# Kernel optimization log

Hardware: AMD Instinct MI355X
Metric: run time of the kernel (lower is better)

The kernel has to match this reference:

```python
import jax, jax.numpy as jnp
import numpy as np

B = 262144          # batch size
NUM_CLASSES = 1000  # number of classes in `classes` dict
CODE_LEN = 512      # length of each binary codeword in class_to_coding


def setup_inputs() -> dict:
    key = jax.random.key(0)
    k1, k2, k3 = jax.random.split(key, 3)
    output = jax.random.randint(k1, (B,), 0, NUM_CLASSES, dtype=jnp.int64 if jax.config.jax_enable_x64 else jnp.int32)
    target = jax.random.randint(k2, (B,), 0, NUM_CLASSES, dtype=output.dtype)
    # classes + class_to_coding fused into one [num_classes, code_len] binary table
    codebook = (jax.random.uniform(k3, (NUM_CLASSES, CODE_LEN)) > 0.5).astype(jnp.float32)
    return {"output": output, "target": target, "codebook": codebook}


def reference(output, target, codebook):
    # Vectorized equivalent of the per-sample Python loop:
    #   dist_i = sum(codebook[pred_i] != codebook[gt_i]); loss = mean_i dist_i
    pred_codes = codebook[output]   # [B, CODE_LEN]
    gt_codes = codebook[target]     # [B, CODE_LEN]
    dists = jnp.sum(pred_codes != gt_codes, axis=-1).astype(jnp.float32)  # [B]
    return jnp.mean(dists)
```

## Files before the change

kernel.cpp:

```cpp
#include <hip/hip_runtime.h>
#include <stdint.h>

#define B_SIZE        262144
#define NUM_CLASSES   1000
#define CODE_LEN      512
#define WORDS_PER_ROW 16
#define PACKED_WORDS  (NUM_CLASSES * WORDS_PER_ROW)
#define CHUNKS        (NUM_CLASSES * 4)
#define HAM_BLOCKS    512
#define SAMPLES_PER_BLOCK (B_SIZE / HAM_BLOCKS)

__global__ __launch_bounds__(256) void pack_kernel(
        const float* __restrict__ codebook,
        uint32_t* __restrict__ packed,
        unsigned long long* __restrict__ accum,
        unsigned int* __restrict__ done) {
    int tid = blockIdx.x * blockDim.x + threadIdx.x;
    if (tid == 0) { *accum = 0ull; *done = 0u; }
    if (tid < NUM_CLASSES * CODE_LEN) {
        float x = codebook[tid];
        unsigned long long m = __ballot(x > 0.5f);
        if ((tid & 31) == 0) {
            packed[tid >> 5] = (uint32_t)(m >> (threadIdx.x & 32));
        }
    }
}

__global__ __launch_bounds__(256) void hamming_kernel(
        const int* __restrict__ output,
        const int* __restrict__ target,
        const uint32_t* __restrict__ packed,
        unsigned long long* __restrict__ accum,
        unsigned int* __restrict__ done,
        float* __restrict__ out) {
    __shared__ uint4 lds[CHUNKS];
    __shared__ unsigned int wsum[4];

    const uint4* pk4 = (const uint4*)packed;
    #pragma unroll
    for (int it = 0; it < 16; it++) {
        int g = threadIdx.x + 256 * it;
        if (g < CHUNKS) {
            int r = g >> 2, k = g & 3;
            lds[(r << 2) + ((k + (r >> 2)) & 3)] = pk4[g];
        }
    }
    __syncthreads();

    int base = blockIdx.x * SAMPLES_PER_BLOCK + threadIdx.x;
    int i0 = base, i1 = base + 256;
    int o0 = output[i0], t0 = target[i0];
    int o1 = output[i1], t1 = target[i1];

    uint4 ao[4], at[4], bo[4], bt[4];
    int so0 = (o0 >> 2) & 3, st0 = (t0 >> 2) & 3;
    int so1 = (o1 >> 2) & 3, st1 = (t1 >> 2) & 3;
    #pragma unroll
    for (int k = 0; k < 4; k++) ao[k] = lds[(o0 << 2) + ((k + so0) & 3)];
    #pragma unroll
    for (int k = 0; k < 4; k++) at[k] = lds[(t0 << 2) + ((k + st0) & 3)];
    #pragma unroll
    for (int k = 0; k < 4; k++) bo[k] = lds[(o1 << 2) + ((k + so1) & 3)];
    #pragma unroll
    for (int k = 0; k < 4; k++) bt[k] = lds[(t1 << 2) + ((k + st1) & 3)];

    unsigned int sum = 0;
    #pragma unroll
    for (int k = 0; k < 4; k++) {
        sum += __popc(ao[k].x ^ at[k].x) + __popc(ao[k].y ^ at[k].y)
             + __popc(ao[k].z ^ at[k].z) + __popc(ao[k].w ^ at[k].w);
        sum += __popc(bo[k].x ^ bt[k].x) + __popc(bo[k].y ^ bt[k].y)
             + __popc(bo[k].z ^ bt[k].z) + __popc(bo[k].w ^ bt[k].w);
    }

    #pragma unroll
    for (int off = 32; off > 0; off >>= 1)
        sum += __shfl_down(sum, off, 64);
    if ((threadIdx.x & 63) == 0)
        wsum[threadIdx.x >> 6] = sum;
    __syncthreads();

    if (threadIdx.x == 0) {
        unsigned int bsum = wsum[0] + wsum[1] + wsum[2] + wsum[3];
        atomicAdd(accum, (unsigned long long)bsum);
        __threadfence();
        unsigned int prev = atomicAdd(done, 1u);
        if (prev == gridDim.x - 1) {
            unsigned long long total = atomicAdd(accum, 0ull);
            out[0] = (float)((double)total / (double)B_SIZE);
        }
    }
}

extern "C" void kernel_launch(void* const* d_in, const int* in_sizes, int n_in,
                              void* d_out, int out_size, void* d_ws, size_t ws_size,
                              hipStream_t stream) {
    const int*   output   = (const int*)d_in[0];
    const int*   target   = (const int*)d_in[1];
    const float* codebook = (const float*)d_in[2];
    float* out = (float*)d_out;

    unsigned long long* accum = (unsigned long long*)d_ws;
    unsigned int* done = (unsigned int*)((char*)d_ws + 8);
    uint32_t* packed = (uint32_t*)((char*)d_ws + 128);

    pack_kernel<<<(NUM_CLASSES * CODE_LEN + 255) / 256, 256, 0, stream>>>(
        codebook, packed, accum, done);
    hamming_kernel<<<HAM_BLOCKS, 256, 0, stream>>>(
        output, target, packed, accum, done, out);
}
```

Baseline: 75.58 us.

## Reduce hamming grid to 128 blocks and replace atomic accumulator with partials

The Hamming kernel now runs 128 blocks, each handling four times as many samples in a loop, so the 64 KB codebook staged into LDS is loaded far fewer times overall. The single 64-bit atomic accumulator is replaced by per-block padded partial slots, and the last block to finish sums them. The trade-off is less parallelism: 128 blocks may not fill all CUs, and each block does a longer serial sweep over its samples.

```diff
diff --git a/kernel.cpp b/kernel.cpp
--- a/kernel.cpp
+++ b/kernel.cpp
@@ -7,16 +7,20 @@
 #define WORDS_PER_ROW 16
 #define PACKED_WORDS  (NUM_CLASSES * WORDS_PER_ROW)
 #define CHUNKS        (NUM_CLASSES * 4)
-#define HAM_BLOCKS    512
+#define HAM_BLOCKS    128
 #define SAMPLES_PER_BLOCK (B_SIZE / HAM_BLOCKS)
+
+#define WS_DONE_OFF     0
+#define WS_PART_OFF     128
+#define WS_PART_STRIDE  32
+#define WS_PACKED_OFF   32768
 
 __global__ __launch_bounds__(256) void pack_kernel(
         const float* __restrict__ codebook,
         uint32_t* __restrict__ packed,
-        unsigned long long* __restrict__ accum,
         unsigned int* __restrict__ done) {
     int tid = blockIdx.x * blockDim.x + threadIdx.x;
-    if (tid == 0) { *accum = 0ull; *done = 0u; }
+    if (tid == 0) *done = 0u;
     if (tid < NUM_CLASSES * CODE_LEN) {
         float x = codebook[tid];
         unsigned long long m = __ballot(x > 0.5f);
@@ -30,11 +34,12 @@
         const int* __restrict__ output,
         const int* __restrict__ target,
         const uint32_t* __restrict__ packed,
-        unsigned long long* __restrict__ accum,
         unsigned int* __restrict__ done,
+        unsigned int* __restrict__ partials,
         float* __restrict__ out) {
     __shared__ uint4 lds[CHUNKS];
     __shared__ unsigned int wsum[4];
+    __shared__ unsigned int last_flag;
 
     const uint4* pk4 = (const uint4*)packed;
     #pragma unroll
@@ -48,29 +53,34 @@
     __syncthreads();
 
     int base = blockIdx.x * SAMPLES_PER_BLOCK + threadIdx.x;
-    int i0 = base, i1 = base + 256;
-    int o0 = output[i0], t0 = target[i0];
-    int o1 = output[i1], t1 = target[i1];
+    unsigned int sum = 0;
 
-    uint4 ao[4], at[4], bo[4], bt[4];
-    int so0 = (o0 >> 2) & 3, st0 = (t0 >> 2) & 3;
-    int so1 = (o1 >> 2) & 3, st1 = (t1 >> 2) & 3;
     #pragma unroll
-    for (int k = 0; k < 4; k++) ao[k] = lds[(o0 << 2) + ((k + so0) & 3)];
-    #pragma unroll
-    for (int k = 0; k < 4; k++) at[k] = lds[(t0 << 2) + ((k + st0) & 3)];
-    #pragma unroll
-    for (int k = 0; k < 4; k++) bo[k] = lds[(o1 << 2) + ((k + so1) & 3)];
-    #pragma unroll
-    for (int k = 0; k < 4; k++) bt[k] = lds[(t1 << 2) + ((k + st1) & 3)];
+    for (int b = 0; b < 4; b++) {
+        int i0 = base + b * 512;
+        int i1 = i0 + 256;
+        int o0 = output[i0], t0 = target[i0];
+        int o1 = output[i1], t1 = target[i1];
 
-    unsigned int sum = 0;
-    #pragma unroll
-    for (int k = 0; k < 4; k++) {
-        sum += __popc(ao[k].x ^ at[k].x) + __popc(ao[k].y ^ at[k].y)
-             + __popc(ao[k].z ^ at[k].z) + __popc(ao[k].w ^ at[k].w);
-        sum += __popc(bo[k].x ^ bt[k].x) + __popc(bo[k].y ^ bt[k].y)
-             + __popc(bo[k].z ^ bt[k].z) + __popc(bo[k].w ^ bt[k].w);
+        uint4 ao[4], at[4], bo[4], bt[4];
+        int so0 = (o0 >> 2) & 3, st0 = (t0 >> 2) & 3;
+        int so1 = (o1 >> 2) & 3, st1 = (t1 >> 2) & 3;
+        #pragma unroll
+        for (int k = 0; k < 4; k++) ao[k] = lds[(o0 << 2) + ((k + so0) & 3)];
+        #pragma unroll
+        for (int k = 0; k < 4; k++) at[k] = lds[(t0 << 2) + ((k + st0) & 3)];
+        #pragma unroll
+        for (int k = 0; k < 4; k++) bo[k] = lds[(o1 << 2) + ((k + so1) & 3)];
+        #pragma unroll
+        for (int k = 0; k < 4; k++) bt[k] = lds[(t1 << 2) + ((k + st1) & 3)];
+
+        #pragma unroll
+        for (int k = 0; k < 4; k++) {
+            sum += __popc(ao[k].x ^ at[k].x) + __popc(ao[k].y ^ at[k].y)
+                 + __popc(ao[k].z ^ at[k].z) + __popc(ao[k].w ^ at[k].w);
+            sum += __popc(bo[k].x ^ bt[k].x) + __popc(bo[k].y ^ bt[k].y)
+                 + __popc(bo[k].z ^ bt[k].z) + __popc(bo[k].w ^ bt[k].w);
+        }
     }
 
     #pragma unroll
@@ -82,11 +92,25 @@
 
     if (threadIdx.x == 0) {
         unsigned int bsum = wsum[0] + wsum[1] + wsum[2] + wsum[3];
-        atomicAdd(accum, (unsigned long long)bsum);
+        atomicExch(&partials[blockIdx.x * WS_PART_STRIDE], bsum);
         __threadfence();
         unsigned int prev = atomicAdd(done, 1u);
-        if (prev == gridDim.x - 1) {
-            unsigned long long total = atomicAdd(accum, 0ull);
+        last_flag = (prev == (unsigned int)(gridDim.x - 1)) ? 1u : 0u;
+    }
+    __syncthreads();
+
+    if (last_flag) {
+        unsigned int v = 0;
+        if (threadIdx.x < HAM_BLOCKS)
+            v = atomicAdd(&partials[threadIdx.x * WS_PART_STRIDE], 0u);
+        #pragma unroll
+        for (int off = 32; off > 0; off >>= 1)
+            v += __shfl_down(v, off, 64);
+        if ((threadIdx.x & 63) == 0)
+            wsum[threadIdx.x >> 6] = v;
+        __syncthreads();
+        if (threadIdx.x == 0) {
+            unsigned long long total = wsum[0] + wsum[1];
             out[0] = (float)((double)total / (double)B_SIZE);
         }
     }
@@ -100,12 +124,12 @@
     const float* codebook = (const float*)d_in[2];
     float* out = (float*)d_out;
 
-    unsigned long long* accum = (unsigned long long*)d_ws;
-    unsigned int* done = (unsigned int*)((char*)d_ws + 8);
-    uint32_t* packed = (uint32_t*)((char*)d_ws + 128);
+    unsigned int* done     = (unsigned int*)((char*)d_ws + WS_DONE_OFF);
+    unsigned int* partials = (unsigned int*)((char*)d_ws + WS_PART_OFF);
+    uint32_t*     packed   = (uint32_t*)((char*)d_ws + WS_PACKED_OFF);
 
     pack_kernel<<<(NUM_CLASSES * CODE_LEN + 255) / 256, 256, 0, stream>>>(
-        codebook, packed, accum, done);
+        codebook, packed, done);
     hamming_kernel<<<HAM_BLOCKS, 256, 0, stream>>>(
-        output, target, packed, accum, done, out);
+        output, target, packed, done, partials, out);
 }
```

After: 66.09 us. 1.14x faster.
